# Performance work log

Hardware: AMD Instinct MI355X
Metric: run time of the kernel (lower is better)

Reference implementation:

```python
import jax, jax.numpy as jnp
import numpy as np

EPS = 1e-5          # InstanceNorm eps (torch default)
KERNEL = 25         # moving_avg_kernel_size
TAU = 1.0           # gumbel softmax temperature
REGIME_NUM = 8


def _inorm(x):
    # InstanceNorm1d without affine on (N, C, L): normalize over last dim (biased var)
    m = x.mean(-1, keepdims=True)
    v = ((x - m) ** 2).mean(-1, keepdims=True)
    return (x - m) * jax.lax.rsqrt(v + EPS)


def _lbr(x, W, b):
    # Linear -> InstanceNorm (over last dim) -> exact GELU
    return jax.nn.gelu(_inorm(x @ W + b), approximate=False)


def _moving_avg(x, k):
    # x: (B, L, C); edge-replicate pad (k-1)//2 on both sides, sliding mean via cumsum
    p = (k - 1) // 2
    xp = jnp.concatenate([jnp.repeat(x[:, :1], p, axis=1), x,
                          jnp.repeat(x[:, -1:], p, axis=1)], axis=1)
    cs = jnp.concatenate([jnp.zeros_like(xp[:, :1]), jnp.cumsum(xp, axis=1)], axis=1)
    return (cs[:, k:] - cs[:, :-k]) / k  # (B, L, C)


def _encode(x, Ws, bs, Wt, bt):
    # inputs - inputs[:, 0:1]; series decomposition; seasonal+trend branches
    x = x - x[:, :1]
    mm = _moving_avg(x, KERNEL)
    return _lbr(x - mm, Ws, bs) + _lbr(mm, Wt, bt)  # (B, L, H)


def reference(inputs_longterm, inputs_shortterm,
              Ws, bs, Wt, bt,
              Wh1, bh1, Wl1, bl1, Wh2, bh2, Wl2, bl2, Wh3, bh3, Wl3, bl3,
              Wr, br, proto):
    e_lt = _encode(inputs_longterm, Ws, bs, Wt, bt)   # (B, L_lt, H)
    e_st = _encode(inputs_shortterm, Ws, bs, Wt, bt)  # (B, L_st, H)

    # RegimeEncoder: alternate hidden-dim and lookback-dim LinearBatchRelu layers
    o = _lbr(e_lt, Wh1, bh1)
    o = jnp.swapaxes(_lbr(jnp.swapaxes(o, 1, 2), Wl1, bl1), 1, 2)
    o = _lbr(o, Wh2, bh2)
    o = jnp.swapaxes(_lbr(jnp.swapaxes(o, 1, 2), Wl2, bl2), 1, 2)
    o = _lbr(o, Wh3, bh3)
    o = jnp.swapaxes(_lbr(jnp.swapaxes(o, 1, 2), Wl3, bl3), 1, 2)  # (B, L_lt//8, H)
    logits = o.reshape(o.shape[0], -1) @ Wr + br  # (B, R)

    # gumbel_softmax(hard=True) with straight-through estimator
    g = jax.random.gumbel(jax.random.key(42), logits.shape, logits.dtype)
    y_soft = jax.nn.softmax((logits + g) / TAU, axis=-1)
    y_hard = jax.nn.one_hot(jnp.argmax(y_soft, axis=-1), REGIME_NUM, dtype=logits.dtype)
    w = y_hard - jax.lax.stop_gradient(y_soft) + y_soft  # (B, R)

    # weighted sum over regime prototypes, then combine with encoded shortterm
    sel = jnp.einsum('br,rnhmo->bnhmo', w, proto)          # (B, L_st, H, M, 3)
    out = jnp.einsum('bnh,bnhmo->bmo', e_st, sel)          # (B, M, 3)
    B = out.shape[0]
    return jax.nn.softmax(out.reshape(B, -1), axis=-1).reshape(out.shape)


def setup_inputs() -> dict:
    key = jax.random.key(0)
    ks = jax.random.split(key, 24)
    B, L_lt, L_st, C, H, R, M = 32, 512, 128, 9, 128, 8, 64
    s = 0.02
    d = {
        'inputs_longterm':  jax.random.normal(ks[0], (B, L_lt, C), jnp.float32),
        'inputs_shortterm': jax.random.normal(ks[1], (B, L_st, C), jnp.float32),
        'Ws': jax.random.normal(ks[2], (C, H), jnp.float32) * s,
        'bs': jnp.zeros((H,), jnp.float32),
        'Wt': jax.random.normal(ks[3], (C, H), jnp.float32) * s,
        'bt': jnp.zeros((H,), jnp.float32),
        'Wh1': jax.random.normal(ks[4], (H, H), jnp.float32) * s,
        'bh1': jnp.zeros((H,), jnp.float32),
        'Wl1': jax.random.normal(ks[5], (L_lt, L_lt // 2), jnp.float32) * s,
        'bl1': jnp.zeros((L_lt // 2,), jnp.float32),
        'Wh2': jax.random.normal(ks[6], (H, H), jnp.float32) * s,
        'bh2': jnp.zeros((H,), jnp.float32),
        'Wl2': jax.random.normal(ks[7], (L_lt // 2, L_lt // 4), jnp.float32) * s,
        'bl2': jnp.zeros((L_lt // 4,), jnp.float32),
        'Wh3': jax.random.normal(ks[8], (H, H), jnp.float32) * s,
        'bh3': jnp.zeros((H,), jnp.float32),
        'Wl3': jax.random.normal(ks[9], (L_lt // 4, L_lt // 8), jnp.float32) * s,
        'bl3': jnp.zeros((L_lt // 8,), jnp.float32),
        'Wr': jax.random.normal(ks[10], (H * L_lt // 8, R), jnp.float32) * s,
        'br': jnp.zeros((R,), jnp.float32),
        'proto': jax.random.normal(ks[11], (R, L_st, H, M, 3), jnp.float32),
    }
    return d
```

## Files before the change

kernel.cpp:

```cpp
#include <hip/hip_runtime.h>
#include <math.h>

#define EPS 1e-5f

__device__ __forceinline__ float gelu_exact(float x) {
    return 0.5f * x * (1.0f + erff(x * 0.7071067811865476f));
}

__device__ float block_sum(float v, float* red) {
    int lane = threadIdx.x & 63, wid = threadIdx.x >> 6;
#pragma unroll
    for (int off = 32; off > 0; off >>= 1) v += __shfl_down(v, off, 64);
    if (lane == 0) red[wid] = v;
    __syncthreads();
    int nw = ((int)blockDim.x + 63) >> 6;
    float s = red[0];
    for (int w = 1; w < nw; w++) s += red[w];
    __syncthreads();
    return s;
}

__device__ float block_max(float v, float* red) {
    int lane = threadIdx.x & 63, wid = threadIdx.x >> 6;
#pragma unroll
    for (int off = 32; off > 0; off >>= 1) v = fmaxf(v, __shfl_down(v, off, 64));
    if (lane == 0) red[wid] = v;
    __syncthreads();
    int nw = ((int)blockDim.x + 63) >> 6;
    float s = red[0];
    for (int w = 1; w < nw; w++) s = fmaxf(s, red[w]);
    __syncthreads();
    return s;
}

__device__ void threefry2x32(unsigned k0, unsigned k1, unsigned x0, unsigned x1,
                             unsigned& o0, unsigned& o1) {
    unsigned ks[3] = {k0, k1, k0 ^ k1 ^ 0x1BD11BDAu};
    const unsigned rot[2][4] = {{13u, 15u, 26u, 6u}, {17u, 29u, 16u, 24u}};
    x0 += ks[0]; x1 += ks[1];
#pragma unroll
    for (int i = 0; i < 5; i++) {
#pragma unroll
        for (int j = 0; j < 4; j++) {
            unsigned r = rot[i & 1][j];
            x0 += x1;
            x1 = (x1 << r) | (x1 >> (32 - r));
            x1 ^= x0;
        }
        x0 += ks[(i + 1) % 3];
        x1 += ks[(i + 2) % 3] + (unsigned)(i + 1);
    }
    o0 = x0; o1 = x1;
}

__device__ float gumbel_at(int j) {
    unsigned o0, o1;
    threefry2x32(0u, 42u, 0u, (unsigned)j, o0, o1);
    unsigned bits = o0 ^ o1;
    float f = __uint_as_float((bits >> 9) | 0x3F800000u) - 1.0f;
    float u = fmaxf(f + 1.17549435e-38f, 1.17549435e-38f);
    return -logf(-logf(u));
}

__device__ void bsum2_128(float& a, float& b, float (*red)[2]) {
    int lane = threadIdx.x & 63, wid = threadIdx.x >> 6;
#pragma unroll
    for (int off = 32; off > 0; off >>= 1) {
        a += __shfl_xor(a, off, 64);
        b += __shfl_xor(b, off, 64);
    }
    if (lane == 0) { red[wid][0] = a; red[wid][1] = b; }
    __syncthreads();
    a = red[0][0] + red[1][0];
    b = red[0][1] + red[1][1];
}

__global__ void encode_kernel(const float* __restrict__ x_lt, const float* __restrict__ x_st,
                              const float* __restrict__ Ws, const float* __restrict__ bs,
                              const float* __restrict__ Wt, const float* __restrict__ bt,
                              float* __restrict__ e_lt, float* __restrict__ e_st) {
    const int H = 128;
    int b = blockIdx.y, t = threadIdx.x;
    const float* x;
    float* e;
    int L, l;
    if (blockIdx.x < 512) { x = x_lt; e = e_lt; L = 512; l = blockIdx.x; }
    else { x = x_st; e = e_st; L = 128; l = blockIdx.x - 512; }
    __shared__ float part[117];
    __shared__ float seas[9], mmv[9];
    __shared__ float redA[2][2], redB[2][2];
    const float* xb = x + (size_t)b * L * 9;
    if (t < 117) {
        int c = t / 13, g = t % 13;
        int lj0 = l + 2 * g - 12;
        lj0 = lj0 < 0 ? 0 : (lj0 >= L ? L - 1 : lj0);
        float s = xb[(size_t)lj0 * 9 + c];
        if (g < 12) {
            int lj1 = l + 2 * g - 11;
            lj1 = lj1 < 0 ? 0 : (lj1 >= L ? L - 1 : lj1);
            s += xb[(size_t)lj1 * 9 + c];
        }
        part[t] = s;
    }
    __syncthreads();
    if (t < 9) {
        float s = 0.f;
        for (int g = 0; g < 13; g++) s += part[t * 13 + g];
        float x0 = xb[t];
        float mm = (s - 25.f * x0) * (1.0f / 25.0f);
        float xd = xb[(size_t)l * 9 + t] - x0;
        mmv[t] = mm;
        seas[t] = xd - mm;
    }
    __syncthreads();
    float ys = bs[t], yt = bt[t];
#pragma unroll
    for (int c = 0; c < 9; c++) {
        ys += seas[c] * Ws[c * H + t];
        yt += mmv[c] * Wt[c * H + t];
    }
    float sa = ys, sb = yt;
    bsum2_128(sa, sb, redA);
    float ms = sa * (1.0f / 128.0f), mt = sb * (1.0f / 128.0f);
    float ds = ys - ms, dt = yt - mt;
    float qa = ds * ds, qb = dt * dt;
    bsum2_128(qa, qb, redB);
    float gy = gelu_exact(ds * rsqrtf(qa * (1.0f / 128.0f) + EPS));
    float gt = gelu_exact(dt * rsqrtf(qb * (1.0f / 128.0f) + EPS));
    e[((size_t)b * L + l) * H + t] = gy + gt;
}

template <int K, int N, int WR, bool TRANS>
__global__ __launch_bounds__(256) void lbr_wave(
    const float* __restrict__ A, int S, int ABOFF,
    const float* __restrict__ W, const float* __restrict__ bias,
    float* __restrict__ out, int OROWS, int OBOFF) {
    constexpr int CG = N / 4;
    constexpr int SG = 64 / CG;
    constexpr int RW = SG * WR;
    constexpr int MT = 4 * RW;
    constexpr int LOG2MT = (MT == 8) ? 3 : ((MT == 16) ? 4 : 5);
    constexpr int STAGE = 4 * RW * K;
    constexpr int TILE = TRANS ? MT * (N + 4) : 0;
    constexpr int LSZ = STAGE > TILE ? STAGE : TILE;
    __shared__ float lds[LSZ];
    const int t = threadIdx.x;
    const int w = t >> 6, ln = t & 63;
    const int sg = ln / CG;
    const int n0 = (ln % CG) * 4;
    const int b = blockIdx.y;
    const int r0b = blockIdx.x * MT;
    const int r0w = r0b + w * RW;
    float* As = lds + w * RW * K;
    const float* Ab = A + (size_t)b * ABOFF;
    for (int idx = ln; idx < RW * (K / 4); idx += 64) {
        int rr = idx / (K / 4), kk = idx % (K / 4);
        float4 v = *(const float4*)(Ab + (size_t)(r0w + rr) * S + kk * 4);
        *(float4*)(As + rr * K + kk * 4) = v;
    }
    float4 acc[WR];
    {
        float4 bv = *(const float4*)(bias + n0);
#pragma unroll
        for (int j = 0; j < WR; j++) acc[j] = bv;
    }
    const float* ap = As + (sg * WR) * K;
    const float* wp = W + n0;
#pragma unroll 2
    for (int k = 0; k < K; k += 4) {
        float4 w0 = *(const float4*)(wp);
        float4 w1 = *(const float4*)(wp + N);
        float4 w2 = *(const float4*)(wp + 2 * N);
        float4 w3 = *(const float4*)(wp + 3 * N);
        wp += 4 * N;
#pragma unroll
        for (int j = 0; j < WR; j++) {
            float4 a4 = *(const float4*)(ap + j * K + k);
            acc[j].x += a4.x * w0.x; acc[j].y += a4.x * w0.y;
            acc[j].z += a4.x * w0.z; acc[j].w += a4.x * w0.w;
            acc[j].x += a4.y * w1.x; acc[j].y += a4.y * w1.y;
            acc[j].z += a4.y * w1.z; acc[j].w += a4.y * w1.w;
            acc[j].x += a4.z * w2.x; acc[j].y += a4.z * w2.y;
            acc[j].z += a4.z * w2.z; acc[j].w += a4.z * w2.w;
            acc[j].x += a4.w * w3.x; acc[j].y += a4.w * w3.y;
            acc[j].z += a4.w * w3.z; acc[j].w += a4.w * w3.w;
        }
    }
    float4 res[WR];
#pragma unroll
    for (int j = 0; j < WR; j++) {
        float s = acc[j].x + acc[j].y + acc[j].z + acc[j].w;
#pragma unroll
        for (int off = CG / 2; off > 0; off >>= 1) s += __shfl_xor(s, off, 64);
        float m = s * (1.0f / (float)N);
        float dx = acc[j].x - m, dy = acc[j].y - m, dz = acc[j].z - m, dw = acc[j].w - m;
        float q = dx * dx + dy * dy + dz * dz + dw * dw;
#pragma unroll
        for (int off = CG / 2; off > 0; off >>= 1) q += __shfl_xor(q, off, 64);
        float inv = rsqrtf(q * (1.0f / (float)N) + EPS);
        res[j].x = gelu_exact(dx * inv);
        res[j].y = gelu_exact(dy * inv);
        res[j].z = gelu_exact(dz * inv);
        res[j].w = gelu_exact(dw * inv);
    }
    if constexpr (TRANS) {
        __syncthreads();
#pragma unroll
        for (int j = 0; j < WR; j++) {
            int rl = w * RW + sg * WR + j;
            *(float4*)(lds + rl * (N + 4) + n0) = res[j];
        }
        __syncthreads();
        float* ob = out + (size_t)b * OBOFF + r0b;
        for (int e = t; e < MT * N; e += 256) {
            int r = e & (MT - 1), n = e >> LOG2MT;
            ob[(size_t)n * OROWS + r] = lds[r * (N + 4) + n];
        }
    } else {
        float* ob = out + (size_t)b * OBOFF;
#pragma unroll
        for (int j = 0; j < WR; j++) {
            int row = r0w + sg * WR + j;
            *(float4*)(ob + (size_t)row * N + n0) = res[j];
        }
    }
}

__global__ __launch_bounds__(256) void logits_select(
    const float* __restrict__ O6, const float* __restrict__ Wr,
    const float* __restrict__ br, float* __restrict__ sel_w, int* __restrict__ sel_r) {
    int b = blockIdx.x, t = threadIdx.x;
    __shared__ float sO6[128 * 68];
    __shared__ float red[4][8];
    const float4* ob4 = (const float4*)(O6 + (size_t)b * 8192);
    for (int i4 = t; i4 < 2048; i4 += 256) {
        float4 v = ob4[i4];
        int p = i4 * 4;
        int h = p >> 6, l4 = p & 63;
        *(float4*)(&sO6[h * 68 + l4]) = v;
    }
    __syncthreads();
    float acc[8] = {0, 0, 0, 0, 0, 0, 0, 0};
#pragma unroll 4
    for (int q = 0; q < 32; q++) {
        int i = q * 256 + t;
        int l4 = i >> 7, h = i & 127;
        float v = sO6[h * 68 + l4];
        const float4* wr = (const float4*)(Wr + (size_t)i * 8);
        float4 w0 = wr[0], w1 = wr[1];
        acc[0] += v * w0.x; acc[1] += v * w0.y; acc[2] += v * w0.z; acc[3] += v * w0.w;
        acc[4] += v * w1.x; acc[5] += v * w1.y; acc[6] += v * w1.z; acc[7] += v * w1.w;
    }
#pragma unroll
    for (int j = 0; j < 8; j++)
#pragma unroll
        for (int off = 32; off > 0; off >>= 1) acc[j] += __shfl_xor(acc[j], off, 64);
    int lane = t & 63, wid = t >> 6;
    if (lane == 0)
        for (int j = 0; j < 8; j++) red[wid][j] = acc[j];
    __syncthreads();
    if (t == 0) {
        float z[8];
        for (int j = 0; j < 8; j++) {
            float lg = br[j] + red[0][j] + red[1][j] + red[2][j] + red[3][j];
            z[j] = lg + gumbel_at(b * 8 + j);
        }
        int am = 0;
        float zm = z[0];
        for (int j = 1; j < 8; j++)
            if (z[j] > zm) { zm = z[j]; am = j; }
        float ssum = 0.f;
        for (int j = 0; j < 8; j++) ssum += expf(z[j] - zm);
        float s = 1.0f / ssum;
        sel_w[b] = (1.0f - s) + s;
        sel_r[b] = am;
    }
}

__global__ void einsum_nsplit(const float* __restrict__ e_st, const float* __restrict__ proto,
                              const int* __restrict__ sel_r, float* __restrict__ part) {
    int n = blockIdx.x, r = blockIdx.y, t = threadIdx.x;
    __shared__ int loc[32];
    __shared__ int s_gs;
    if (t == 0) {
        int g = 0;
        for (int bb = 0; bb < 32; bb++)
            if (sel_r[bb] == r) loc[g++] = bb;
        s_gs = g;
    }
    __syncthreads();
    int gs = s_gs;
    if (gs == 0) return;
    __shared__ float es[8][128];
    const float* pb = proto + ((size_t)r * 128 + n) * 128 * 192;
    for (int s0 = 0; s0 < gs; s0 += 8) {
        int np = gs - s0 < 8 ? gs - s0 : 8;
        __syncthreads();
        for (int i4 = t; i4 < 256; i4 += 192) {
            int sb = i4 >> 5, h4 = i4 & 31;
            float4 v = make_float4(0.f, 0.f, 0.f, 0.f);
            if (sb < np) {
                int b = loc[s0 + sb];
                v = ((const float4*)(e_st + ((size_t)b * 128 + n) * 128))[h4];
            }
            *(float4*)(&es[sb][h4 * 4]) = v;
        }
        __syncthreads();
        float a0 = 0.f, a1 = 0.f, a2 = 0.f, a3 = 0.f;
        float a4 = 0.f, a5 = 0.f, a6 = 0.f, a7 = 0.f;
#pragma unroll 8
        for (int h = 0; h < 128; h++) {
            float p = pb[h * 192 + t];
            a0 += es[0][h] * p; a1 += es[1][h] * p;
            a2 += es[2][h] * p; a3 += es[3][h] * p;
            a4 += es[4][h] * p; a5 += es[5][h] * p;
            a6 += es[6][h] * p; a7 += es[7][h] * p;
        }
        float av[8] = {a0, a1, a2, a3, a4, a5, a6, a7};
#pragma unroll
        for (int sb = 0; sb < 8; sb++) {
            if (sb < np) {
                int b = loc[s0 + sb];
                part[((size_t)b * 128 + n) * 192 + t] = av[sb];
            }
        }
    }
}

__global__ void finalize_kernel(const float* __restrict__ part, const float* __restrict__ sel_w,
                                float* __restrict__ out) {
    int b = blockIdx.x, t = threadIdx.x;
    __shared__ float red[4];
    float v = 0.f;
#pragma unroll 8
    for (int c = 0; c < 128; c++) v += part[((size_t)b * 128 + c) * 192 + t];
    v *= sel_w[b];
    float mx = block_max(v, red);
    float e = expf(v - mx);
    float s = block_sum(e, red);
    out[(size_t)b * 192 + t] = e / s;
}

extern "C" void kernel_launch(void* const* d_in, const int* in_sizes, int n_in,
                              void* d_out, int out_size, void* d_ws, size_t ws_size,
                              hipStream_t stream) {
    const float* in_lt = (const float*)d_in[0];
    const float* in_st = (const float*)d_in[1];
    const float* Ws  = (const float*)d_in[2];  const float* bs  = (const float*)d_in[3];
    const float* Wt  = (const float*)d_in[4];  const float* bt  = (const float*)d_in[5];
    const float* Wh1 = (const float*)d_in[6];  const float* bh1 = (const float*)d_in[7];
    const float* Wl1 = (const float*)d_in[8];  const float* bl1 = (const float*)d_in[9];
    const float* Wh2 = (const float*)d_in[10]; const float* bh2 = (const float*)d_in[11];
    const float* Wl2 = (const float*)d_in[12]; const float* bl2 = (const float*)d_in[13];
    const float* Wh3 = (const float*)d_in[14]; const float* bh3 = (const float*)d_in[15];
    const float* Wl3 = (const float*)d_in[16]; const float* bl3 = (const float*)d_in[17];
    const float* Wr  = (const float*)d_in[18]; const float* br  = (const float*)d_in[19];
    const float* proto = (const float*)d_in[20];
    float* out = (float*)d_out;

    float* ws = (float*)d_ws;
    size_t off = 0;
    float* e_lt = ws + off; off += (size_t)32 * 512 * 128;
    float* e_st = ws + off; off += (size_t)32 * 128 * 128;
    float* O1T = ws + off; off += (size_t)128 * 16384;
    float* O2T = ws + off; off += (size_t)256 * 4096;
    float* O3T = ws + off; off += (size_t)128 * 8192;
    float* O4T = ws + off; off += (size_t)128 * 4096;
    float* O5T = ws + off; off += (size_t)128 * 4096;
    float* O6 = ws + off; off += (size_t)32 * 128 * 64;
    float* part = ws + off; off += (size_t)32 * 128 * 192;
    float* sel_w = ws + off; off += 32;
    int* sel_r = (int*)(ws + off); off += 32;

    encode_kernel<<<dim3(640, 32), 128, 0, stream>>>(in_lt, in_st, Ws, bs, Wt, bt, e_lt, e_st);
    lbr_wave<128, 128, 2, true><<<dim3(1024, 1), 256, 0, stream>>>(
        e_lt, 128, 0, Wh1, bh1, O1T, 16384, 0);
    lbr_wave<512, 256, 2, true><<<dim3(16, 32), 256, 0, stream>>>(
        O1T, 16384, 512, Wl1, bl1, O2T, 4096, 128);
    lbr_wave<128, 128, 2, true><<<dim3(16, 32), 256, 0, stream>>>(
        O2T, 4096, 128, Wh2, bh2, O3T, 8192, 256);
    lbr_wave<256, 128, 1, true><<<dim3(16, 32), 256, 0, stream>>>(
        O3T, 8192, 256, Wl2, bl2, O4T, 4096, 128);
    lbr_wave<128, 128, 1, true><<<dim3(16, 32), 256, 0, stream>>>(
        O4T, 4096, 128, Wh3, bh3, O5T, 4096, 128);
    lbr_wave<128, 64, 1, false><<<dim3(8, 32), 256, 0, stream>>>(
        O5T, 4096, 128, Wl3, bl3, O6, 0, 8192);
    logits_select<<<32, 256, 0, stream>>>(O6, Wr, br, sel_w, sel_r);
    einsum_nsplit<<<dim3(128, 8), 192, 0, stream>>>(e_st, proto, sel_r, part);
    finalize_kernel<<<32, 192, 0, stream>>>(part, sel_w, out);
}
```

Measured before the change: 363.4 us.

## Restructure encode to wave-per-row, enlarge LBR row tiles, two n per einsum block

```diff
diff --git a/kernel.cpp b/kernel.cpp
--- a/kernel.cpp
+++ b/kernel.cpp
@@ -62,72 +62,72 @@
     return -logf(-logf(u));
 }
 
-__device__ void bsum2_128(float& a, float& b, float (*red)[2]) {
-    int lane = threadIdx.x & 63, wid = threadIdx.x >> 6;
+__global__ __launch_bounds__(256) void encode_kernel(
+    const float* __restrict__ x_lt, const float* __restrict__ x_st,
+    const float* __restrict__ Ws, const float* __restrict__ bs,
+    const float* __restrict__ Wt, const float* __restrict__ bt,
+    float* __restrict__ e_lt, float* __restrict__ e_st) {
+    const int b = blockIdx.y;
+    const int w = threadIdx.x >> 6, ln = threadIdx.x & 63;
+    const float* x; float* e; int L, l;
+    if (blockIdx.x < 128) { x = x_lt; e = e_lt; L = 512; l = blockIdx.x * 4 + w; }
+    else { x = x_st; e = e_st; L = 128; l = (blockIdx.x - 128) * 4 + w; }
+    __shared__ float xw_all[4][228];
+    __shared__ float sm_all[4][20];
+    float* xw = xw_all[w];
+    float* sm = sm_all[w];
+    const float* xb = x + (size_t)b * L * 9;
+#pragma unroll
+    for (int q = 0; q < 4; q++) {
+        int f = ln + 64 * q;
+        if (f < 225) {
+            int row = f / 9, c = f - row * 9;
+            int rr = l - 12 + row;
+            rr = rr < 0 ? 0 : (rr >= L ? L - 1 : rr);
+            xw[f] = xb[(size_t)rr * 9 + c];
+        }
+    }
+    __syncthreads();
+    if (ln < 9) {
+        float s = 0.f;
+#pragma unroll
+        for (int j = 0; j < 25; j++) s += xw[j * 9 + ln];
+        float x0 = xb[ln];
+        float mm = (s - 25.f * x0) * (1.0f / 25.0f);
+        sm[ln] = (xw[108 + ln] - x0) - mm;
+        sm[ln + 10] = mm;
+    }
+    __syncthreads();
+    float ysA = bs[ln], ysB = bs[ln + 64];
+    float ytA = bt[ln], ytB = bt[ln + 64];
+#pragma unroll
+    for (int c = 0; c < 9; c++) {
+        float sv = sm[c], mv = sm[c + 10];
+        ysA += sv * Ws[c * 128 + ln];
+        ysB += sv * Ws[c * 128 + ln + 64];
+        ytA += mv * Wt[c * 128 + ln];
+        ytB += mv * Wt[c * 128 + ln + 64];
+    }
+    float sa = ysA + ysB, sb2 = ytA + ytB;
 #pragma unroll
     for (int off = 32; off > 0; off >>= 1) {
-        a += __shfl_xor(a, off, 64);
-        b += __shfl_xor(b, off, 64);
-    }
-    if (lane == 0) { red[wid][0] = a; red[wid][1] = b; }
-    __syncthreads();
-    a = red[0][0] + red[1][0];
-    b = red[0][1] + red[1][1];
-}
-
-__global__ void encode_kernel(const float* __restrict__ x_lt, const float* __restrict__ x_st,
-                              const float* __restrict__ Ws, const float* __restrict__ bs,
-                              const float* __restrict__ Wt, const float* __restrict__ bt,
-                              float* __restrict__ e_lt, float* __restrict__ e_st) {
-    const int H = 128;
-    int b = blockIdx.y, t = threadIdx.x;
-    const float* x;
-    float* e;
-    int L, l;
-    if (blockIdx.x < 512) { x = x_lt; e = e_lt; L = 512; l = blockIdx.x; }
-    else { x = x_st; e = e_st; L = 128; l = blockIdx.x - 512; }
-    __shared__ float part[117];
-    __shared__ float seas[9], mmv[9];
-    __shared__ float redA[2][2], redB[2][2];
-    const float* xb = x + (size_t)b * L * 9;
-    if (t < 117) {
-        int c = t / 13, g = t % 13;
-        int lj0 = l + 2 * g - 12;
-        lj0 = lj0 < 0 ? 0 : (lj0 >= L ? L - 1 : lj0);
-        float s = xb[(size_t)lj0 * 9 + c];
-        if (g < 12) {
-            int lj1 = l + 2 * g - 11;
-            lj1 = lj1 < 0 ? 0 : (lj1 >= L ? L - 1 : lj1);
-            s += xb[(size_t)lj1 * 9 + c];
-        }
-        part[t] = s;
-    }
-    __syncthreads();
-    if (t < 9) {
-        float s = 0.f;
-        for (int g = 0; g < 13; g++) s += part[t * 13 + g];
-        float x0 = xb[t];
-        float mm = (s - 25.f * x0) * (1.0f / 25.0f);
-        float xd = xb[(size_t)l * 9 + t] - x0;
-        mmv[t] = mm;
-        seas[t] = xd - mm;
-    }
-    __syncthreads();
-    float ys = bs[t], yt = bt[t];
-#pragma unroll
-    for (int c = 0; c < 9; c++) {
-        ys += seas[c] * Ws[c * H + t];
-        yt += mmv[c] * Wt[c * H + t];
-    }
-    float sa = ys, sb = yt;
-    bsum2_128(sa, sb, redA);
-    float ms = sa * (1.0f / 128.0f), mt = sb * (1.0f / 128.0f);
-    float ds = ys - ms, dt = yt - mt;
-    float qa = ds * ds, qb = dt * dt;
-    bsum2_128(qa, qb, redB);
-    float gy = gelu_exact(ds * rsqrtf(qa * (1.0f / 128.0f) + EPS));
-    float gt = gelu_exact(dt * rsqrtf(qb * (1.0f / 128.0f) + EPS));
-    e[((size_t)b * L + l) * H + t] = gy + gt;
+        sa += __shfl_xor(sa, off, 64);
+        sb2 += __shfl_xor(sb2, off, 64);
+    }
+    float ms = sa * (1.0f / 128.0f), mt = sb2 * (1.0f / 128.0f);
+    float dA = ysA - ms, dB = ysB - ms;
+    float tA = ytA - mt, tB = ytB - mt;
+    float qa = dA * dA + dB * dB, qb = tA * tA + tB * tB;
+#pragma unroll
+    for (int off = 32; off > 0; off >>= 1) {
+        qa += __shfl_xor(qa, off, 64);
+        qb += __shfl_xor(qb, off, 64);
+    }
+    float inva = rsqrtf(qa * (1.0f / 128.0f) + EPS);
+    float invb = rsqrtf(qb * (1.0f / 128.0f) + EPS);
+    float* eo = e + ((size_t)b * L + l) * 128;
+    eo[ln] = gelu_exact(dA * inva) + gelu_exact(tA * invb);
+    eo[ln + 64] = gelu_exact(dB * inva) + gelu_exact(tB * invb);
 }
 
 template <int K, int N, int WR, bool TRANS>
@@ -143,7 +143,7 @@
     constexpr int STAGE = 4 * RW * K;
     constexpr int TILE = TRANS ? MT * (N + 4) : 0;
     constexpr int LSZ = STAGE > TILE ? STAGE : TILE;
-    __shared__ float lds[LSZ];
+    __shared__ __align__(16) float lds[LSZ];
     const int t = threadIdx.x;
     const int w = t >> 6, ln = t & 63;
     const int sg = ln / CG;
@@ -277,9 +277,10 @@
     }
 }
 
-__global__ void einsum_nsplit(const float* __restrict__ e_st, const float* __restrict__ proto,
-                              const int* __restrict__ sel_r, float* __restrict__ part) {
-    int n = blockIdx.x, r = blockIdx.y, t = threadIdx.x;
+__global__ __launch_bounds__(192) void einsum_nsplit(
+    const float* __restrict__ e_st, const float* __restrict__ proto,
+    const int* __restrict__ sel_r, float* __restrict__ part) {
+    const int n0 = blockIdx.x * 2, r = blockIdx.y, t = threadIdx.x;
     __shared__ int loc[32];
     __shared__ int s_gs;
     if (t == 0) {
@@ -289,39 +290,49 @@
         s_gs = g;
     }
     __syncthreads();
-    int gs = s_gs;
+    const int gs = s_gs;
     if (gs == 0) return;
-    __shared__ float es[8][128];
-    const float* pb = proto + ((size_t)r * 128 + n) * 128 * 192;
+    __shared__ __align__(16) float es[2][8][128];
+    const float* pb0 = proto + ((size_t)r * 128 + n0) * (128 * 192) + t;
+    const float* pb1 = pb0 + 128 * 192;
     for (int s0 = 0; s0 < gs; s0 += 8) {
         int np = gs - s0 < 8 ? gs - s0 : 8;
         __syncthreads();
-        for (int i4 = t; i4 < 256; i4 += 192) {
-            int sb = i4 >> 5, h4 = i4 & 31;
+        for (int i4 = t; i4 < 512; i4 += 192) {
+            int nn = i4 >> 8, rem = i4 & 255;
+            int sb = rem >> 5, h4 = rem & 31;
             float4 v = make_float4(0.f, 0.f, 0.f, 0.f);
             if (sb < np) {
-                int b = loc[s0 + sb];
-                v = ((const float4*)(e_st + ((size_t)b * 128 + n) * 128))[h4];
+                int bb = loc[s0 + sb];
+                v = ((const float4*)(e_st + ((size_t)bb * 128 + n0 + nn) * 128))[h4];
             }
-            *(float4*)(&es[sb][h4 * 4]) = v;
+            *(float4*)(&es[nn][sb][h4 * 4]) = v;
         }
         __syncthreads();
-        float a0 = 0.f, a1 = 0.f, a2 = 0.f, a3 = 0.f;
-        float a4 = 0.f, a5 = 0.f, a6 = 0.f, a7 = 0.f;
-#pragma unroll 8
-        for (int h = 0; h < 128; h++) {
-            float p = pb[h * 192 + t];
-            a0 += es[0][h] * p; a1 += es[1][h] * p;
-            a2 += es[2][h] * p; a3 += es[3][h] * p;
-            a4 += es[4][h] * p; a5 += es[5][h] * p;
-            a6 += es[6][h] * p; a7 += es[7][h] * p;
-        }
-        float av[8] = {a0, a1, a2, a3, a4, a5, a6, a7};
+        float a0[8] = {0, 0, 0, 0, 0, 0, 0, 0};
+        float a1[8] = {0, 0, 0, 0, 0, 0, 0, 0};
+#pragma unroll 2
+        for (int h = 0; h < 128; h += 4) {
+            float p00 = pb0[(h + 0) * 192], p01 = pb0[(h + 1) * 192];
+            float p02 = pb0[(h + 2) * 192], p03 = pb0[(h + 3) * 192];
+            float p10 = pb1[(h + 0) * 192], p11 = pb1[(h + 1) * 192];
+            float p12 = pb1[(h + 2) * 192], p13 = pb1[(h + 3) * 192];
+#pragma unroll
+            for (int sb = 0; sb < 8; sb++) {
+                float4 e0 = *(const float4*)(&es[0][sb][h]);
+                float4 e1 = *(const float4*)(&es[1][sb][h]);
+                a0[sb] += e0.x * p00; a0[sb] += e0.y * p01;
+                a0[sb] += e0.z * p02; a0[sb] += e0.w * p03;
+                a1[sb] += e1.x * p10; a1[sb] += e1.y * p11;
+                a1[sb] += e1.z * p12; a1[sb] += e1.w * p13;
+            }
+        }
 #pragma unroll
         for (int sb = 0; sb < 8; sb++) {
             if (sb < np) {
-                int b = loc[s0 + sb];
-                part[((size_t)b * 128 + n) * 192 + t] = av[sb];
+                int bb = loc[s0 + sb];
+                part[((size_t)bb * 128 + n0) * 192 + t] = a0[sb];
+                part[((size_t)bb * 128 + n0 + 1) * 192 + t] = a1[sb];
             }
         }
     }
@@ -372,20 +383,20 @@
     float* sel_w = ws + off; off += 32;
     int* sel_r = (int*)(ws + off); off += 32;
 
-    encode_kernel<<<dim3(640, 32), 128, 0, stream>>>(in_lt, in_st, Ws, bs, Wt, bt, e_lt, e_st);
-    lbr_wave<128, 128, 2, true><<<dim3(1024, 1), 256, 0, stream>>>(
+    encode_kernel<<<dim3(160, 32), 256, 0, stream>>>(in_lt, in_st, Ws, bs, Wt, bt, e_lt, e_st);
+    lbr_wave<128, 128, 4, true><<<dim3(512, 1), 256, 0, stream>>>(
         e_lt, 128, 0, Wh1, bh1, O1T, 16384, 0);
-    lbr_wave<512, 256, 2, true><<<dim3(16, 32), 256, 0, stream>>>(
+    lbr_wave<512, 256, 4, true><<<dim3(8, 32), 256, 0, stream>>>(
         O1T, 16384, 512, Wl1, bl1, O2T, 4096, 128);
-    lbr_wave<128, 128, 2, true><<<dim3(16, 32), 256, 0, stream>>>(
+    lbr_wave<128, 128, 4, true><<<dim3(8, 32), 256, 0, stream>>>(
         O2T, 4096, 128, Wh2, bh2, O3T, 8192, 256);
-    lbr_wave<256, 128, 1, true><<<dim3(16, 32), 256, 0, stream>>>(
+    lbr_wave<256, 128, 2, true><<<dim3(8, 32), 256, 0, stream>>>(
         O3T, 8192, 256, Wl2, bl2, O4T, 4096, 128);
-    lbr_wave<128, 128, 1, true><<<dim3(16, 32), 256, 0, stream>>>(
+    lbr_wave<128, 128, 2, true><<<dim3(8, 32), 256, 0, stream>>>(
         O4T, 4096, 128, Wh3, bh3, O5T, 4096, 128);
     lbr_wave<128, 64, 1, false><<<dim3(8, 32), 256, 0, stream>>>(
         O5T, 4096, 128, Wl3, bl3, O6, 0, 8192);
     logits_select<<<32, 256, 0, stream>>>(O6, Wr, br, sel_w, sel_r);
-    einsum_nsplit<<<dim3(128, 8), 192, 0, stream>>>(e_st, proto, sel_r, part);
+    einsum_nsplit<<<dim3(64, 8), 192, 0, stream>>>(e_st, proto, sel_r, part);
     finalize_kernel<<<32, 192, 0, stream>>>(part, sel_w, out);
 }
```

Measured after the change: 377.2 us. +3.8%, slower.
